# Kernel optimization log

Measured on AMD Instinct MI355X. Metric: run time of the kernel, lower is better.

## Reference

```python
import jax, jax.numpy as jnp
import numpy as np

B = 16384          # batch_size
NL = 4096          # nb_labels
T = 64             # max_num_trials


def setup_inputs() -> dict:
    key = jax.random.key(0)
    k1, k2 = jax.random.split(key)
    inputs = jax.random.normal(k1, (B, NL), dtype=jnp.float32)
    # targets are one-hot (original code takes argmax to find the single positive)
    labels = jax.random.randint(k2, (B,), 0, NL)
    targets = jax.nn.one_hot(labels, NL, dtype=jnp.float32)
    return {"inputs": inputs, "targets": targets}


def _warp_forward(inputs, targets, max_num_trials=T, sample_key=jax.random.key(42)):
    # Sequential uniform sampling WITHOUT replacement from the remaining negative
    # set == walking a uniform random permutation of the negatives. We realize the
    # permutation with iid uniform noise + argsort, then find the first trial whose
    # margin is > 0 (the while-loop exit condition).
    bsz, nb_labels = inputs.shape
    pos_idx = jnp.argmax(targets, axis=1)                                  # [B]
    pos_score = jnp.take_along_axis(inputs, pos_idx[:, None], axis=1)      # [B,1]

    noise = jax.random.uniform(sample_key, (bsz, nb_labels))               # [B,NL]
    # force the positive label to sort last so the first NL-1 slots are negatives
    noise = noise.at[jnp.arange(bsz), pos_idx].set(-1.0)
    order = jnp.argsort(-noise, axis=1)[:, :max_num_trials]                # [B,T] random negative order

    neg_scores = jnp.take_along_axis(inputs, order, axis=1)                # [B,T]
    margins = 1.0 + neg_scores - pos_score                                 # [B,T]

    hit = margins > 0.0
    found = jnp.any(hit, axis=1)                                           # [B]
    first = jnp.argmax(hit, axis=1)                                        # first trial with margin>0
    num_trials = jnp.where(found, first + 1, max_num_trials)               # [B]
    pick_col = jnp.where(found, first, max_num_trials - 1)
    neg_idx = jnp.take_along_axis(order, pick_col[:, None], axis=1)[:, 0]  # [B]
    # original: after the loop, set loss unless final margin < 0
    set_flag = found | (margins[:, -1] >= 0.0)                             # [B]

    loss_weight = jnp.log(jnp.floor((nb_labels - 1.0) / num_trials.astype(jnp.float32)))
    L = jnp.where(set_flag, loss_weight, 0.0)                              # [B]

    neg_onehot = jnp.zeros_like(inputs).at[jnp.arange(bsz), neg_idx].add(
        set_flag.astype(inputs.dtype))                                     # [B,NL]

    loss = L * (1.0 - jnp.sum(targets * inputs, axis=1)
                + jnp.sum(neg_onehot * inputs, axis=1))                    # [B]
    return jnp.sum(loss, axis=0, keepdims=True)                            # [1]


def reference(inputs, targets):
    return _warp_forward(inputs, targets)
```

## Files before the change

kernel.cpp:

```cpp
#include <hip/hip_runtime.h>
#include <stdint.h>

#define NLBL      4096
#define HALF_ROWS 8192
#define HALF_CNT  33554432u
#define TPB       512

__device__ __forceinline__ uint32_t rotl32(uint32_t x, uint32_t r) {
    return __builtin_amdgcn_alignbit(x, x, 32u - r);
}

__device__ __forceinline__ void threefry2x32(uint32_t x0, uint32_t x1,
                                             uint32_t& o0, uint32_t& o1) {
    const uint32_t ks0 = 0u;
    const uint32_t ks1 = 42u;
    const uint32_t ks2 = 0x1BD11BDAu ^ ks0 ^ ks1;
    x0 += ks0; x1 += ks1;
#define TF_RND(r) x0 += x1; x1 = rotl32(x1, (r)); x1 ^= x0;
    TF_RND(13u) TF_RND(15u) TF_RND(26u) TF_RND(6u)
    x0 += ks1; x1 += ks2 + 1u;
    TF_RND(17u) TF_RND(29u) TF_RND(16u) TF_RND(24u)
    x0 += ks2; x1 += ks0 + 2u;
    TF_RND(13u) TF_RND(15u) TF_RND(26u) TF_RND(6u)
    x0 += ks0; x1 += ks1 + 3u;
    TF_RND(17u) TF_RND(29u) TF_RND(16u) TF_RND(24u)
    x0 += ks1; x1 += ks2 + 4u;
    TF_RND(13u) TF_RND(15u) TF_RND(26u) TF_RND(6u)
    x0 += ks2; x1 += ks0 + 5u;
#undef TF_RND
    o0 = x0; o1 = x1;
}


__global__ void __launch_bounds__(TPB)
warp_loss_main(const float* __restrict__ inputs,
               const float* __restrict__ targets,
               float* __restrict__ part)
{
    const int b   = blockIdx.x;
    const int tid = threadIdx.x;
    const size_t r0 = (size_t)b * NLBL;
    const size_t r1 = (size_t)(b + HALF_ROWS) * NLBL;

    const float4* in0 = reinterpret_cast<const float4*>(inputs  + r0);
    const float4* in1 = reinterpret_cast<const float4*>(inputs  + r1);
    const float4* tg0 = reinterpret_cast<const float4*>(targets + r0);
    const float4* tg1 = reinterpret_cast<const float4*>(targets + r1);

    __shared__ float              s_sc[2][NLBL];
    __shared__ int                s_pos[2];
    __shared__ unsigned long long s_key[2][8];
    __shared__ unsigned int       s_cnt[8];

    uint32_t ub0[8], ub1[8];
    const uint32_t cbase0 = (uint32_t)b * NLBL;

    const int v4a = tid;
    const int v4b = tid + 512;
    const float4 a0A = in0[v4a];
    const float4 a0B = in0[v4b];
    const float4 a1A = in1[v4a];
    const float4 a1B = in1[v4b];
    const float4 t0A = tg0[v4a];
    const float4 t0B = tg0[v4b];
    const float4 t1A = tg1[v4a];
    const float4 t1B = tg1[v4b];

    #pragma unroll
    for (int kc = 0; kc < 2; ++kc) {
        const int c = (tid + (kc << 9)) << 2;
        #pragma unroll
        for (int j = 0; j < 4; ++j) {
            const uint32_t i = cbase0 + (uint32_t)(c + j);
            uint32_t o0, o1;
            threefry2x32(i, i + HALF_CNT, o0, o1);
            ub0[kc*4+j] = o0 >> 9;
            ub1[kc*4+j] = o1 >> 9;
        }
    }

    reinterpret_cast<float4*>(s_sc[0])[v4a] = a0A;
    reinterpret_cast<float4*>(s_sc[0])[v4b] = a0B;
    reinterpret_cast<float4*>(s_sc[1])[v4a] = a1A;
    reinterpret_cast<float4*>(s_sc[1])[v4b] = a1B;

    {
        const int cA = v4a << 2, cB = v4b << 2;
        if (t0A.x > 0.5f || t0A.y > 0.5f || t0A.z > 0.5f || t0A.w > 0.5f)
            s_pos[0] = cA + (t0A.x > 0.5f ? 0 : (t0A.y > 0.5f ? 1 : (t0A.z > 0.5f ? 2 : 3)));
        if (t0B.x > 0.5f || t0B.y > 0.5f || t0B.z > 0.5f || t0B.w > 0.5f)
            s_pos[0] = cB + (t0B.x > 0.5f ? 0 : (t0B.y > 0.5f ? 1 : (t0B.z > 0.5f ? 2 : 3)));
        if (t1A.x > 0.5f || t1A.y > 0.5f || t1A.z > 0.5f || t1A.w > 0.5f)
            s_pos[1] = cA + (t1A.x > 0.5f ? 0 : (t1A.y > 0.5f ? 1 : (t1A.z > 0.5f ? 2 : 3)));
        if (t1B.x > 0.5f || t1B.y > 0.5f || t1B.z > 0.5f || t1B.w > 0.5f)
            s_pos[1] = cB + (t1B.x > 0.5f ? 0 : (t1B.y > 0.5f ? 1 : (t1B.z > 0.5f ? 2 : 3)));
    }
    __syncthreads();

    const int   pos0 = s_pos[0],       pos1 = s_pos[1];
    const float psc0 = s_sc[0][pos0];
    const float psc1 = s_sc[1][pos1];

    unsigned long long key0 = 0ull, key1 = 0ull;
    #pragma unroll
    for (int kc = 0; kc < 2; ++kc) {
        const int v4 = tid + (kc << 9);
        const float4 x0 = reinterpret_cast<const float4*>(s_sc[0])[v4];
        const float4 x1 = reinterpret_cast<const float4*>(s_sc[1])[v4];
        const float q0[4] = { x0.x, x0.y, x0.z, x0.w };
        const float q1[4] = { x1.x, x1.y, x1.z, x1.w };
        #pragma unroll
        for (int j = 0; j < 4; ++j) {
            const int c = (v4 << 2) + j;
            const int k = kc*4 + j;
            const float m0 = (1.0f + q0[j]) - psc0;
            const float m1 = (1.0f + q1[j]) - psc1;
            if (c != pos0 && m0 > 0.0f) {
                const unsigned long long kk =
                    ((unsigned long long)(ub0[k] + 1u) << 12) | (unsigned long long)(4095 - c);
                if (kk > key0) key0 = kk;
            }
            if (c != pos1 && m1 > 0.0f) {
                const unsigned long long kk =
                    ((unsigned long long)(ub1[k] + 1u) << 12) | (unsigned long long)(4095 - c);
                if (kk > key1) key1 = kk;
            }
        }
    }
    #pragma unroll
    for (int off = 32; off; off >>= 1) {
        const unsigned long long q0 = __shfl_xor(key0, off);
        const unsigned long long q1 = __shfl_xor(key1, off);
        if (q0 > key0) key0 = q0;
        if (q1 > key1) key1 = q1;
    }
    const int wv = tid >> 6;
    if ((tid & 63) == 0) { s_key[0][wv] = key0; s_key[1][wv] = key1; }
    __syncthreads();

    unsigned long long kk0 = s_key[0][0], kk1 = s_key[1][0];
    #pragma unroll
    for (int w = 1; w < 8; ++w) {
        if (s_key[0][w] > kk0) kk0 = s_key[0][w];
        if (s_key[1][w] > kk1) kk1 = s_key[1][w];
    }
    const int      c0  = (kk0 == 0ull) ? -1 : 4095 - (int)(kk0 & 0xFFFull);
    const int      c1  = (kk1 == 0ull) ? -1 : 4095 - (int)(kk1 & 0xFFFull);
    const uint32_t nb0 = (kk0 == 0ull) ? 0xFFFFFFFFu : (uint32_t)(kk0 >> 12) - 1u;
    const uint32_t nb1 = (kk1 == 0ull) ? 0xFFFFFFFFu : (uint32_t)(kk1 >> 12) - 1u;

    uint32_t cnt = 0;
    #pragma unroll
    for (int k = 0; k < 8; ++k) {
        const int c = (tid << 2) + ((k >> 2) << 11) + (k & 3);
        if (c0 >= 0 && c != pos0 && (ub0[k] > nb0 || (ub0[k] == nb0 && c < c0))) cnt += 1u;
        if (c1 >= 0 && c != pos1 && (ub1[k] > nb1 || (ub1[k] == nb1 && c < c1))) cnt += 1u << 16;
    }
    #pragma unroll
    for (int off = 32; off; off >>= 1) cnt += __shfl_xor(cnt, off);
    if ((tid & 63) == 0) s_cnt[wv] = cnt;
    __syncthreads();

    if (tid == 0) {
        uint32_t tot = 0;
        #pragma unroll
        for (int w = 0; w < 8; ++w) tot += s_cnt[w];
        const int rank0 = (int)(tot & 0xFFFFu);
        const int rank1 = (int)(tot >> 16);
        float total = 0.0f;
        if (c0 >= 0 && rank0 < 64) {
            const float margin = (1.0f - psc0) + s_sc[0][c0];
            total += logf(floorf(4095.0f / (float)(rank0 + 1))) * margin;
        }
        if (c1 >= 0 && rank1 < 64) {
            const float margin = (1.0f - psc1) + s_sc[1][c1];
            total += logf(floorf(4095.0f / (float)(rank1 + 1))) * margin;
        }
        part[b] = total;
    }
}

__global__ void __launch_bounds__(1024)
warp_loss_reduce(const float* __restrict__ part, float* __restrict__ out)
{
    const int tid = threadIdx.x;
    const float4 a = reinterpret_cast<const float4*>(part)[tid];
    const float4 b = reinterpret_cast<const float4*>(part)[tid + 1024];
    float s = ((a.x + a.y) + (a.z + a.w)) + ((b.x + b.y) + (b.z + b.w));
    #pragma unroll
    for (int off = 32; off; off >>= 1) s += __shfl_xor(s, off);
    __shared__ float sm[16];
    if ((tid & 63) == 0) sm[tid >> 6] = s;
    __syncthreads();
    if (tid == 0) {
        float t = 0.0f;
        #pragma unroll
        for (int w = 0; w < 16; ++w) t += sm[w];
        out[0] = t;
    }
}

extern "C" void kernel_launch(void* const* d_in, const int* in_sizes, int n_in,
                              void* d_out, int out_size, void* d_ws, size_t ws_size,
                              hipStream_t stream) {
    const float* inputs  = (const float*)d_in[0];
    const float* targets = (const float*)d_in[1];
    float* out  = (float*)d_out;
    float* part = (float*)d_ws;

    warp_loss_main  <<<dim3(HALF_ROWS), dim3(TPB),  0, stream>>>(inputs, targets, part);
    warp_loss_reduce<<<dim3(1),         dim3(1024), 0, stream>>>(part, out);
}
```

Baseline: 520.2 us.

## Persistent grid with register prefetch of next row pair, drop LDS score staging

Launches a smaller grid where each block loops over four row pairs, issuing global loads for the next pair before processing the current one. Scores stay in registers instead of being staged in shared memory, and the chosen negative's score is passed through a small shared slot. Barriers become a raw s_barrier after an LDS waitcnt, and the per-thread max uses 32-bit compares. This costs more registers for the prefetch buffers and fewer blocks to spread load imbalance.

```diff
diff --git a/kernel.cpp b/kernel.cpp
--- a/kernel.cpp
+++ b/kernel.cpp
@@ -5,6 +5,8 @@
 #define HALF_ROWS 8192
 #define HALF_CNT  33554432u
 #define TPB       512
+#define GRID      2048
+#define ITERS     4
 
 __device__ __forceinline__ uint32_t rotl32(uint32_t x, uint32_t r) {
     return __builtin_amdgcn_alignbit(x, x, 32u - r);
@@ -31,152 +33,169 @@
     o0 = x0; o1 = x1;
 }
 
+#define LBAR() do { asm volatile("s_waitcnt lgkmcnt(0)" ::: "memory"); \
+                    __builtin_amdgcn_s_barrier(); } while (0)
+
 
 __global__ void __launch_bounds__(TPB)
 warp_loss_main(const float* __restrict__ inputs,
                const float* __restrict__ targets,
                float* __restrict__ part)
 {
-    const int b   = blockIdx.x;
     const int tid = threadIdx.x;
-    const size_t r0 = (size_t)b * NLBL;
-    const size_t r1 = (size_t)(b + HALF_ROWS) * NLBL;
-
-    const float4* in0 = reinterpret_cast<const float4*>(inputs  + r0);
-    const float4* in1 = reinterpret_cast<const float4*>(inputs  + r1);
-    const float4* tg0 = reinterpret_cast<const float4*>(targets + r0);
-    const float4* tg1 = reinterpret_cast<const float4*>(targets + r1);
-
-    __shared__ float              s_sc[2][NLBL];
+    const int wv  = tid >> 6;
+    const int v4a = tid, v4b = tid + 512;
+
     __shared__ int                s_pos[2];
+    __shared__ float              s_psc[2];
     __shared__ unsigned long long s_key[2][8];
     __shared__ unsigned int       s_cnt[8];
-
-    uint32_t ub0[8], ub1[8];
-    const uint32_t cbase0 = (uint32_t)b * NLBL;
-
-    const int v4a = tid;
-    const int v4b = tid + 512;
-    const float4 a0A = in0[v4a];
-    const float4 a0B = in0[v4b];
-    const float4 a1A = in1[v4a];
-    const float4 a1B = in1[v4b];
-    const float4 t0A = tg0[v4a];
-    const float4 t0B = tg0[v4b];
-    const float4 t1A = tg1[v4a];
-    const float4 t1B = tg1[v4b];
+    __shared__ float              s_star[2];
+
+    float4 a0A, a0B, a1A, a1B, t0A, t0B, t1A, t1B;
+    {
+        const int rp = blockIdx.x;
+        const float4* i0 = reinterpret_cast<const float4*>(inputs  + (size_t)rp * NLBL);
+        const float4* i1 = reinterpret_cast<const float4*>(inputs  + (size_t)(rp + HALF_ROWS) * NLBL);
+        const float4* g0 = reinterpret_cast<const float4*>(targets + (size_t)rp * NLBL);
+        const float4* g1 = reinterpret_cast<const float4*>(targets + (size_t)(rp + HALF_ROWS) * NLBL);
+        a0A = i0[v4a]; a0B = i0[v4b]; a1A = i1[v4a]; a1B = i1[v4b];
+        t0A = g0[v4a]; t0B = g0[v4b]; t1A = g1[v4a]; t1B = g1[v4b];
+    }
 
     #pragma unroll
-    for (int kc = 0; kc < 2; ++kc) {
-        const int c = (tid + (kc << 9)) << 2;
-        #pragma unroll
-        for (int j = 0; j < 4; ++j) {
-            const uint32_t i = cbase0 + (uint32_t)(c + j);
-            uint32_t o0, o1;
-            threefry2x32(i, i + HALF_CNT, o0, o1);
-            ub0[kc*4+j] = o0 >> 9;
-            ub1[kc*4+j] = o1 >> 9;
-        }
-    }
-
-    reinterpret_cast<float4*>(s_sc[0])[v4a] = a0A;
-    reinterpret_cast<float4*>(s_sc[0])[v4b] = a0B;
-    reinterpret_cast<float4*>(s_sc[1])[v4a] = a1A;
-    reinterpret_cast<float4*>(s_sc[1])[v4b] = a1B;
-
-    {
-        const int cA = v4a << 2, cB = v4b << 2;
-        if (t0A.x > 0.5f || t0A.y > 0.5f || t0A.z > 0.5f || t0A.w > 0.5f)
-            s_pos[0] = cA + (t0A.x > 0.5f ? 0 : (t0A.y > 0.5f ? 1 : (t0A.z > 0.5f ? 2 : 3)));
-        if (t0B.x > 0.5f || t0B.y > 0.5f || t0B.z > 0.5f || t0B.w > 0.5f)
-            s_pos[0] = cB + (t0B.x > 0.5f ? 0 : (t0B.y > 0.5f ? 1 : (t0B.z > 0.5f ? 2 : 3)));
-        if (t1A.x > 0.5f || t1A.y > 0.5f || t1A.z > 0.5f || t1A.w > 0.5f)
-            s_pos[1] = cA + (t1A.x > 0.5f ? 0 : (t1A.y > 0.5f ? 1 : (t1A.z > 0.5f ? 2 : 3)));
-        if (t1B.x > 0.5f || t1B.y > 0.5f || t1B.z > 0.5f || t1B.w > 0.5f)
-            s_pos[1] = cB + (t1B.x > 0.5f ? 0 : (t1B.y > 0.5f ? 1 : (t1B.z > 0.5f ? 2 : 3)));
-    }
-    __syncthreads();
-
-    const int   pos0 = s_pos[0],       pos1 = s_pos[1];
-    const float psc0 = s_sc[0][pos0];
-    const float psc1 = s_sc[1][pos1];
-
-    unsigned long long key0 = 0ull, key1 = 0ull;
-    #pragma unroll
-    for (int kc = 0; kc < 2; ++kc) {
-        const int v4 = tid + (kc << 9);
-        const float4 x0 = reinterpret_cast<const float4*>(s_sc[0])[v4];
-        const float4 x1 = reinterpret_cast<const float4*>(s_sc[1])[v4];
-        const float q0[4] = { x0.x, x0.y, x0.z, x0.w };
-        const float q1[4] = { x1.x, x1.y, x1.z, x1.w };
-        #pragma unroll
-        for (int j = 0; j < 4; ++j) {
-            const int c = (v4 << 2) + j;
-            const int k = kc*4 + j;
-            const float m0 = (1.0f + q0[j]) - psc0;
-            const float m1 = (1.0f + q1[j]) - psc1;
+    for (int it = 0; it < ITERS; ++it) {
+        const int rp = blockIdx.x + it * GRID;
+        const uint32_t cbase = (uint32_t)rp * NLBL;
+
+        const float sc0[8] = { a0A.x, a0A.y, a0A.z, a0A.w, a0B.x, a0B.y, a0B.z, a0B.w };
+        const float sc1[8] = { a1A.x, a1A.y, a1A.z, a1A.w, a1B.x, a1B.y, a1B.z, a1B.w };
+
+        uint32_t ub0[8], ub1[8];
+        #pragma unroll
+        for (int kc = 0; kc < 2; ++kc) {
+            #pragma unroll
+            for (int j = 0; j < 4; ++j) {
+                const uint32_t i = cbase + (uint32_t)((tid << 2) + j + (kc << 11));
+                uint32_t o0, o1;
+                threefry2x32(i, i + HALF_CNT, o0, o1);
+                ub0[kc*4+j] = o0 >> 9;
+                ub1[kc*4+j] = o1 >> 9;
+            }
+        }
+
+        {
+            const int cA = v4a << 2, cB = v4b << 2;
+            const float tg0v[8] = { t0A.x, t0A.y, t0A.z, t0A.w, t0B.x, t0B.y, t0B.z, t0B.w };
+            const float tg1v[8] = { t1A.x, t1A.y, t1A.z, t1A.w, t1B.x, t1B.y, t1B.z, t1B.w };
+            int   idx0 = -1, idx1 = -1;
+            float val0 = 0.0f, val1 = 0.0f;
+            #pragma unroll
+            for (int k = 0; k < 8; ++k) {
+                const int c = (k < 4) ? (cA + k) : (cB + (k - 4));
+                const bool h0 = tg0v[k] > 0.5f;
+                const bool h1 = tg1v[k] > 0.5f;
+                idx0 = h0 ? c : idx0;  val0 = h0 ? sc0[k] : val0;
+                idx1 = h1 ? c : idx1;  val1 = h1 ? sc1[k] : val1;
+            }
+            if (idx0 >= 0) { s_pos[0] = idx0; s_psc[0] = val0; }
+            if (idx1 >= 0) { s_pos[1] = idx1; s_psc[1] = val1; }
+        }
+
+        float4 na0A, na0B, na1A, na1B, nt0A, nt0B, nt1A, nt1B;
+        if (it + 1 < ITERS) {
+            const int nrp = rp + GRID;
+            const float4* i0 = reinterpret_cast<const float4*>(inputs  + (size_t)nrp * NLBL);
+            const float4* i1 = reinterpret_cast<const float4*>(inputs  + (size_t)(nrp + HALF_ROWS) * NLBL);
+            const float4* g0 = reinterpret_cast<const float4*>(targets + (size_t)nrp * NLBL);
+            const float4* g1 = reinterpret_cast<const float4*>(targets + (size_t)(nrp + HALF_ROWS) * NLBL);
+            na0A = i0[v4a]; na0B = i0[v4b]; na1A = i1[v4a]; na1B = i1[v4b];
+            nt0A = g0[v4a]; nt0B = g0[v4b]; nt1A = g1[v4a]; nt1B = g1[v4b];
+        }
+
+        LBAR();
+
+        const int   pos0 = s_pos[0], pos1 = s_pos[1];
+        const float psc0 = s_psc[0], psc1 = s_psc[1];
+
+        uint32_t bu0 = 0, bc0 = 0, bu1 = 0, bc1 = 0;
+        #pragma unroll
+        for (int k = 0; k < 8; ++k) {
+            const int c = (tid << 2) + (k & 3) + ((k >= 4) ? 2048 : 0);
+            const float m0 = (1.0f + sc0[k]) - psc0;
+            const float m1 = (1.0f + sc1[k]) - psc1;
             if (c != pos0 && m0 > 0.0f) {
-                const unsigned long long kk =
-                    ((unsigned long long)(ub0[k] + 1u) << 12) | (unsigned long long)(4095 - c);
-                if (kk > key0) key0 = kk;
+                const uint32_t u = ub0[k] + 1u;
+                if (u > bu0) { bu0 = u; bc0 = (uint32_t)c; }
             }
             if (c != pos1 && m1 > 0.0f) {
-                const unsigned long long kk =
-                    ((unsigned long long)(ub1[k] + 1u) << 12) | (unsigned long long)(4095 - c);
-                if (kk > key1) key1 = kk;
-            }
-        }
-    }
-    #pragma unroll
-    for (int off = 32; off; off >>= 1) {
-        const unsigned long long q0 = __shfl_xor(key0, off);
-        const unsigned long long q1 = __shfl_xor(key1, off);
-        if (q0 > key0) key0 = q0;
-        if (q1 > key1) key1 = q1;
-    }
-    const int wv = tid >> 6;
-    if ((tid & 63) == 0) { s_key[0][wv] = key0; s_key[1][wv] = key1; }
-    __syncthreads();
-
-    unsigned long long kk0 = s_key[0][0], kk1 = s_key[1][0];
-    #pragma unroll
-    for (int w = 1; w < 8; ++w) {
-        if (s_key[0][w] > kk0) kk0 = s_key[0][w];
-        if (s_key[1][w] > kk1) kk1 = s_key[1][w];
-    }
-    const int      c0  = (kk0 == 0ull) ? -1 : 4095 - (int)(kk0 & 0xFFFull);
-    const int      c1  = (kk1 == 0ull) ? -1 : 4095 - (int)(kk1 & 0xFFFull);
-    const uint32_t nb0 = (kk0 == 0ull) ? 0xFFFFFFFFu : (uint32_t)(kk0 >> 12) - 1u;
-    const uint32_t nb1 = (kk1 == 0ull) ? 0xFFFFFFFFu : (uint32_t)(kk1 >> 12) - 1u;
-
-    uint32_t cnt = 0;
-    #pragma unroll
-    for (int k = 0; k < 8; ++k) {
-        const int c = (tid << 2) + ((k >> 2) << 11) + (k & 3);
-        if (c0 >= 0 && c != pos0 && (ub0[k] > nb0 || (ub0[k] == nb0 && c < c0))) cnt += 1u;
-        if (c1 >= 0 && c != pos1 && (ub1[k] > nb1 || (ub1[k] == nb1 && c < c1))) cnt += 1u << 16;
-    }
-    #pragma unroll
-    for (int off = 32; off; off >>= 1) cnt += __shfl_xor(cnt, off);
-    if ((tid & 63) == 0) s_cnt[wv] = cnt;
-    __syncthreads();
-
-    if (tid == 0) {
-        uint32_t tot = 0;
-        #pragma unroll
-        for (int w = 0; w < 8; ++w) tot += s_cnt[w];
-        const int rank0 = (int)(tot & 0xFFFFu);
-        const int rank1 = (int)(tot >> 16);
-        float total = 0.0f;
-        if (c0 >= 0 && rank0 < 64) {
-            const float margin = (1.0f - psc0) + s_sc[0][c0];
-            total += logf(floorf(4095.0f / (float)(rank0 + 1))) * margin;
-        }
-        if (c1 >= 0 && rank1 < 64) {
-            const float margin = (1.0f - psc1) + s_sc[1][c1];
-            total += logf(floorf(4095.0f / (float)(rank1 + 1))) * margin;
-        }
-        part[b] = total;
+                const uint32_t u = ub1[k] + 1u;
+                if (u > bu1) { bu1 = u; bc1 = (uint32_t)c; }
+            }
+        }
+        unsigned long long key0 = bu0 ? (((unsigned long long)bu0 << 12) |
+                                         (unsigned long long)(4095u - bc0)) : 0ull;
+        unsigned long long key1 = bu1 ? (((unsigned long long)bu1 << 12) |
+                                         (unsigned long long)(4095u - bc1)) : 0ull;
+        #pragma unroll
+        for (int off = 32; off; off >>= 1) {
+            const unsigned long long q0 = __shfl_xor(key0, off);
+            const unsigned long long q1 = __shfl_xor(key1, off);
+            if (q0 > key0) key0 = q0;
+            if (q1 > key1) key1 = q1;
+        }
+        if ((tid & 63) == 0) { s_key[0][wv] = key0; s_key[1][wv] = key1; }
+
+        LBAR();
+
+        unsigned long long kk0 = s_key[0][0], kk1 = s_key[1][0];
+        #pragma unroll
+        for (int w = 1; w < 8; ++w) {
+            if (s_key[0][w] > kk0) kk0 = s_key[0][w];
+            if (s_key[1][w] > kk1) kk1 = s_key[1][w];
+        }
+        const int      c0  = (kk0 == 0ull) ? -1 : 4095 - (int)(kk0 & 0xFFFull);
+        const int      c1  = (kk1 == 0ull) ? -1 : 4095 - (int)(kk1 & 0xFFFull);
+        const uint32_t nb0 = (kk0 == 0ull) ? 0xFFFFFFFFu : (uint32_t)(kk0 >> 12) - 1u;
+        const uint32_t nb1 = (kk1 == 0ull) ? 0xFFFFFFFFu : (uint32_t)(kk1 >> 12) - 1u;
+
+        uint32_t cnt = 0;
+        #pragma unroll
+        for (int k = 0; k < 8; ++k) {
+            const int c = (tid << 2) + (k & 3) + ((k >= 4) ? 2048 : 0);
+            if (c0 >= 0 && c != pos0 && (ub0[k] > nb0 || (ub0[k] == nb0 && c < c0))) cnt += 1u;
+            if (c1 >= 0 && c != pos1 && (ub1[k] > nb1 || (ub1[k] == nb1 && c < c1))) cnt += 1u << 16;
+            if (c == c0) s_star[0] = sc0[k];
+            if (c == c1) s_star[1] = sc1[k];
+        }
+        #pragma unroll
+        for (int off = 32; off; off >>= 1) cnt += __shfl_xor(cnt, off);
+        if ((tid & 63) == 0) s_cnt[wv] = cnt;
+
+        LBAR();
+
+        if (tid == 0) {
+            uint32_t tot = 0;
+            #pragma unroll
+            for (int w = 0; w < 8; ++w) tot += s_cnt[w];
+            const int rank0 = (int)(tot & 0xFFFFu);
+            const int rank1 = (int)(tot >> 16);
+            float total = 0.0f;
+            if (c0 >= 0 && rank0 < 64) {
+                const float margin = (1.0f - psc0) + s_star[0];
+                total += logf(floorf(4095.0f / (float)(rank0 + 1))) * margin;
+            }
+            if (c1 >= 0 && rank1 < 64) {
+                const float margin = (1.0f - psc1) + s_star[1];
+                total += logf(floorf(4095.0f / (float)(rank1 + 1))) * margin;
+            }
+            part[rp] = total;
+        }
+
+        if (it + 1 < ITERS) {
+            a0A = na0A; a0B = na0B; a1A = na1A; a1B = na1B;
+            t0A = nt0A; t0B = nt0B; t1A = nt1A; t1B = nt1B;
+        }
     }
 }
 
@@ -208,6 +227,6 @@
     float* out  = (float*)d_out;
     float* part = (float*)d_ws;
 
-    warp_loss_main  <<<dim3(HALF_ROWS), dim3(TPB),  0, stream>>>(inputs, targets, part);
-    warp_loss_reduce<<<dim3(1),         dim3(1024), 0, stream>>>(part, out);
-}
+    warp_loss_main  <<<dim3(GRID), dim3(TPB),  0, stream>>>(inputs, targets, part);
+    warp_loss_reduce<<<dim3(1),    dim3(1024), 0, stream>>>(part, out);
+}
```

After: 531.7 us. +2.2%, slower.
